# Performance work log

Hardware: AMD Instinct MI355X
Metric: run time of the kernel (lower is better)

## Reference

```python
import jax, jax.numpy as jnp
import numpy as np

NMS_THR = 0.3


def pairwise_iou(b):
    # b: [N,4] in x1,y1,x2,y2
    area = (b[:, 2] - b[:, 0]) * (b[:, 3] - b[:, 1])  # [N]
    x1 = jnp.maximum(b[:, None, 0], b[None, :, 0])
    y1 = jnp.maximum(b[:, None, 1], b[None, :, 1])
    x2 = jnp.minimum(b[:, None, 2], b[None, :, 2])
    y2 = jnp.minimum(b[:, None, 3], b[None, :, 3])
    inter = jnp.clip(x2 - x1, 0.0) * jnp.clip(y2 - y1, 0.0)
    return inter / (area[:, None] + area[None, :] - inter + 1e-9)


def nms_keep(boxes, scores, valid, thr):
    # greedy NMS, fixed-shape: returns bool keep mask in original order
    N = boxes.shape[0]
    order = jnp.argsort(-jnp.where(valid, scores, -jnp.inf))
    b = boxes[order]
    v = valid[order]
    iou = pairwise_iou(b)  # [N,N]

    def step(keep, i):
        suppressed = jnp.any(keep & (iou[i] > thr))
        keep = keep.at[i].set(v[i] & jnp.logical_not(suppressed))
        return keep, None

    keep_sorted, _ = jax.lax.scan(step, jnp.zeros((N,), dtype=bool), jnp.arange(N))
    return jnp.zeros((N,), dtype=bool).at[order].set(keep_sorted)


def setup_inputs() -> dict:
    key = jax.random.key(0)
    k1, k2, k3, k4 = jax.random.split(key, 4)
    N, C, S = 6000, 81, 800
    # well-formed proposals: x1,y1 in [0, 600), w,h in [8, 200)
    xy = jax.random.uniform(k1, (N, 2), dtype=jnp.float32) * 600.0
    wh = 8.0 + jax.random.uniform(k2, (N, 2), dtype=jnp.float32) * 192.0
    proposals = jnp.concatenate([xy, xy + wh], axis=1)  # [N,4]
    reg = jax.random.normal(k3, (N, C * 4), dtype=jnp.float32)
    clss = jax.random.normal(k4, (N, C), dtype=jnp.float32) * 2.0
    stds = jnp.array([0.1, 0.1, 0.2, 0.2], dtype=jnp.float32)
    return {"proposals": proposals, "reg": reg, "clss": clss, "stds": stds, "img_size": S}


def reference(proposals, reg, clss, stds, img_size):
    N, C = clss.shape
    # anchors_bbox2offset: x1y1x2y2 -> center x,y + w,h
    w = proposals[:, 2] - proposals[:, 0]
    h = proposals[:, 3] - proposals[:, 1]
    cx = proposals[:, 0] + 0.5 * w
    cy = proposals[:, 1] + 0.5 * h
    # class selection
    probs = jax.nn.softmax(clss, axis=1)
    cls_idx = jnp.argmax(probs, axis=1)  # [N]
    score = jnp.take_along_axis(probs, cls_idx[:, None], axis=1)[:, 0]
    valid = cls_idx != 0  # non-background
    reg4 = reg.reshape(N, C, 4)
    t = jnp.take_along_axis(reg4, cls_idx[:, None, None], axis=1)[:, 0, :] * stds  # [N,4]
    # decode
    px = cx + w * t[:, 0]
    py = cy + h * t[:, 1]
    pw = w * jnp.exp(t[:, 2])
    ph = h * jnp.exp(t[:, 3])
    # offset2bbox + clip
    hi = jnp.float32(img_size - 1)
    x1 = jnp.clip(px - 0.5 * pw, 0.0, hi)
    y1 = jnp.clip(py - 0.5 * ph, 0.0, hi)
    x2 = jnp.clip(px + 0.5 * pw, 0.0, hi)
    y2 = jnp.clip(py + 0.5 * ph, 0.0, hi)
    boxes = jnp.stack((x1, y1, x2, y2), axis=1)  # [N,4]
    keep = nms_keep(jax.lax.stop_gradient(boxes), jax.lax.stop_gradient(score), valid, NMS_THR)
    m = keep.astype(boxes.dtype)
    return boxes * m[:, None], score * m, cls_idx * keep.astype(cls_idx.dtype)
```

## Files before the change

### kernel.cpp

```cpp
#include <hip/hip_runtime.h>
#include <math.h>

#define NMS_THR 0.3f
#define NACC 8

__device__ __forceinline__ float fmul(float a, float b){ return __fmul_rn(a,b); }
__device__ __forceinline__ float fadd(float a, float b){ return __fadd_rn(a,b); }
__device__ __forceinline__ float fsub(float a, float b){ return __fsub_rn(a,b); }

#define BAR_LDS() asm volatile("s_waitcnt lgkmcnt(0)\n\ts_barrier" ::: "memory")

__device__ __forceinline__ unsigned long long rdlane64(unsigned long long v, int a) {
    unsigned long long l = (unsigned int)__builtin_amdgcn_readlane((int)(unsigned int)v, a);
    unsigned long long h = (unsigned int)__builtin_amdgcn_readlane((int)(unsigned int)(v >> 32), a);
    return (h << 32) | l;
}
__device__ __forceinline__ unsigned long long rfl64(unsigned long long x){
    unsigned int lo = (unsigned int)__builtin_amdgcn_readfirstlane((int)(unsigned int)x);
    unsigned int hi = (unsigned int)__builtin_amdgcn_readfirstlane((int)(unsigned int)(x >> 32));
    return ((unsigned long long)hi << 32) | lo;
}

__global__ __launch_bounds__(256) void k_decode(
    const float* __restrict__ prop, const float* __restrict__ reg,
    const float* __restrict__ clss, const float* __restrict__ stds,
    const int* __restrict__ imgsz,
    float* __restrict__ boxes, float* __restrict__ key,
    float* __restrict__ score, int* __restrict__ cls,
    int N, int C)
{
    int wid  = threadIdx.x >> 6;
    int lane = threadIdx.x & 63;
    int n = blockIdx.x * 4 + wid;
    if (n >= N) return;
    const float* row = clss + (long)n * C;
    float ninf = -__builtin_inff();
    float x0 = (lane < C)      ? row[lane]      : ninf;
    float x1 = (lane + 64 < C) ? row[lane + 64] : ninf;
    float m = fmaxf(x0, x1);
    for (int o = 32; o > 0; o >>= 1) m = fmaxf(m, __shfl_xor(m, o));
    float e0 = (lane < C)      ? expf(x0 - m) : 0.0f;
    float e1 = (lane + 64 < C) ? expf(x1 - m) : 0.0f;
    float s = e0 + e1;
    for (int o = 32; o > 0; o >>= 1) s += __shfl_xor(s, o);
    float bv; int bi;
    if (e0 >= e1) { bv = e0; bi = lane; } else { bv = e1; bi = lane + 64; }
    for (int o = 32; o > 0; o >>= 1) {
        float ov = __shfl_xor(bv, o);
        int   oi = __shfl_xor(bi, o);
        if (ov > bv || (ov == bv && oi < bi)) { bv = ov; bi = oi; }
    }
    if (lane == 0) {
        float sc = 1.0f / s;
        int   c  = bi;
        int   valid = (c != 0);
        float p0 = prop[n*4+0], p1 = prop[n*4+1], p2 = prop[n*4+2], p3 = prop[n*4+3];
        float w  = fsub(p2, p0), h = fsub(p3, p1);
        float cx = fadd(p0, fmul(0.5f, w));
        float cy = fadd(p1, fmul(0.5f, h));
        const float* rr = reg + (long)n * C * 4 + (long)c * 4;
        float t0 = fmul(rr[0], stds[0]);
        float t1 = fmul(rr[1], stds[1]);
        float t2 = fmul(rr[2], stds[2]);
        float t3 = fmul(rr[3], stds[3]);
        float px = fadd(cx, fmul(w, t0));
        float py = fadd(cy, fmul(h, t1));
        float pw = fmul(w, expf(t2));
        float ph = fmul(h, expf(t3));
        float hi = (float)(imgsz[0] - 1);
        float bx1 = fminf(fmaxf(fsub(px, fmul(0.5f, pw)), 0.0f), hi);
        float by1 = fminf(fmaxf(fsub(py, fmul(0.5f, ph)), 0.0f), hi);
        float bx2 = fminf(fmaxf(fadd(px, fmul(0.5f, pw)), 0.0f), hi);
        float by2 = fminf(fmaxf(fadd(py, fmul(0.5f, ph)), 0.0f), hi);
        boxes[n*4+0]=bx1; boxes[n*4+1]=by1; boxes[n*4+2]=bx2; boxes[n*4+3]=by2;
        score[n] = sc;
        cls[n]   = c;
        key[n]   = valid ? sc : ninf;
    }
}

__global__ __launch_bounds__(256) void k_rank(
    const float* __restrict__ key, const float* __restrict__ boxes,
    float* __restrict__ boxesSorted, float* __restrict__ areaSorted,
    float* __restrict__ keySorted, int* __restrict__ rank,
    int* __restrict__ nValidPtr, int N)
{
    extern __shared__ float lkey[];
    __shared__ int part[256];
    int tid = threadIdx.x;
    for (int j = tid; j < N; j += 256) lkey[j] = key[j];
    __syncthreads();

    int i = blockIdx.x * 64 + (tid & 63);
    int s = tid >> 6;
    int Q = (N + 3) >> 2;
    int r_part = 0;
    if (i < N) {
        float ki = lkey[i];
        int j0 = s * Q, j1 = min(N, j0 + Q);
        for (int j = j0; j < j1; ++j) {
            float kj = lkey[j];
            r_part += (kj > ki) || (kj == ki && j < i);
        }
    }
    part[tid] = r_part;
    __syncthreads();

    if (tid < 64 && i < N) {
        int r = part[tid] + part[tid+64] + part[tid+128] + part[tid+192];
        float ki = lkey[i];
        rank[i] = r;
        float b0 = boxes[i*4+0], b1 = boxes[i*4+1], b2 = boxes[i*4+2], b3 = boxes[i*4+3];
        boxesSorted[r*4+0]=b0; boxesSorted[r*4+1]=b1; boxesSorted[r*4+2]=b2; boxesSorted[r*4+3]=b3;
        areaSorted[r] = fmul(fsub(b2,b0), fsub(b3,b1));
        keySorted[r]  = ki;
    }

    if (blockIdx.x == 0) {
        __syncthreads();
        float ninf = -__builtin_inff();
        int inv = 0;
        for (int j = tid; j < N; j += 256) inv += (lkey[j] == ninf);
        part[tid] = inv;
        __syncthreads();
        if (tid == 0) {
            int t = 0;
            for (int q = 0; q < 256; ++q) t += part[q];
            nValidPtr[0] = N - t;
        }
    }
}

__global__ __launch_bounds__(256) void k_mask(
    const float* __restrict__ bs, const float* __restrict__ areas,
    const float* __restrict__ keySorted, unsigned long long* __restrict__ mask,
    unsigned long long* __restrict__ dq,
    int N, int W, int Wpad)
{
    int wid  = threadIdx.x >> 6;
    int lane = threadIdx.x & 63;
    int i = blockIdx.x * 4 + wid;
    if (i >= N) return;
    if (keySorted[i] == -__builtin_inff()) return;
    float ax1 = bs[i*4+0], ay1 = bs[i*4+1], ax2 = bs[i*4+2], ay2 = bs[i*4+3];
    float aa  = areas[i];
    int w0 = i >> 6;
    if (lane == 0) {
        dq[i*4+0] = 0ULL; dq[i*4+1] = 0ULL; dq[i*4+2] = 0ULL; dq[i*4+3] = 0ULL;
    }
    for (int w = w0; w < W; ++w) {
        int j = w*64 + lane;
        int bit = 0;
        if (j < N && j > i) {
            float bx1 = bs[j*4+0], by1 = bs[j*4+1], bx2 = bs[j*4+2], by2 = bs[j*4+3];
            float ba  = areas[j];
            float ix1 = fmaxf(ax1,bx1), iy1 = fmaxf(ay1,by1);
            float ix2 = fminf(ax2,bx2), iy2 = fminf(ay2,by2);
            float iw = fmaxf(fsub(ix2,ix1), 0.0f);
            float ih = fmaxf(fsub(iy2,iy1), 0.0f);
            float inter = fmul(iw, ih);
            float denom = fadd(fsub(fadd(aa, ba), inter), 1e-9f);
            float iou = inter / denom;
            bit = (iou > NMS_THR) ? 1 : 0;
        }
        unsigned long long bm = __ballot(bit);
        if (lane == 0) {
            mask[(long)i*Wpad + w] = bm;
            int d = w - w0;
            if (d < 4) dq[i*4+d] = bm;
        }
    }
}

__global__ __launch_bounds__((NACC+1)*64, 1) void k_scan(
    const unsigned long long* __restrict__ mask,
    const unsigned long long* __restrict__ dq,
    const int* __restrict__ nValidPtr,
    int* __restrict__ keepSorted, int N, int W, int Wpad)
{
    __shared__ unsigned long long ldsPartA[NACC+1];
    __shared__ unsigned long long ldsPartB[NACC+1];
    __shared__ unsigned long long ldsKeepLo, ldsKeepHi;
    int tid  = threadIdx.x;
    int wid  = tid >> 6;
    int lane = tid & 63;
    for (int i = tid; i < N; i += (NACC+1)*64) keepSorted[i] = 0;
    if (tid <= NACC) { ldsPartA[tid] = 0ULL; ldsPartB[tid] = 0ULL; }
    if (tid == 0) { ldsKeepLo = 0ULL; ldsKeepHi = 0ULL; }
    __syncthreads();

    int nValid  = __builtin_amdgcn_readfirstlane(nValidPtr[0]);
    int nChunks = (nValid + 127) >> 7;

    unsigned long long A0=0,A1=0,A2=0,A3=0,B0=0,B1=0,B2=0,B3=0;
    unsigned long long sacc_prevA = 0ULL, sacc_prevB = 0ULL;
    if (wid == 0) {
        int rA = lane, rB = 64 + lane;
        if (rA < N && nChunks > 0) {
            ulonglong2 a01 = *(const ulonglong2*)(dq + (size_t)rA*4);
            ulonglong2 a23 = *(const ulonglong2*)(dq + (size_t)rA*4 + 2);
            A0=a01.x; A1=a01.y; A2=a23.x; A3=a23.y;
        }
        if (rB < N && nChunks > 0) {
            ulonglong2 b01 = *(const ulonglong2*)(dq + (size_t)rB*4);
            ulonglong2 b23 = *(const ulonglong2*)(dq + (size_t)rB*4 + 2);
            B0=b01.x; B1=b01.y; B2=b23.x; B3=b23.y;
        }
    }
    unsigned long long accx = 0ULL, accy = 0ULL;
    bool accWave = (wid >= 1);
    int  accIdx  = wid - 1;
    bool laneok  = (2*lane + 1 < Wpad);

    for (int c = 0; c < nChunks; ++c) {
        int base = c << 7;
        if (wid == 0) {
            unsigned long long nA0=0,nA1=0,nA2=0,nA3=0,nB0=0,nB1=0,nB2=0,nB3=0;
            if (c + 1 < nChunks) {
                int rA = base + 128 + lane, rB = base + 192 + lane;
                if (rA < N) {
                    ulonglong2 a01 = *(const ulonglong2*)(dq + (size_t)rA*4);
                    ulonglong2 a23 = *(const ulonglong2*)(dq + (size_t)rA*4 + 2);
                    nA0=a01.x; nA1=a01.y; nA2=a23.x; nA3=a23.y;
                }
                if (rB < N) {
                    ulonglong2 b01 = *(const ulonglong2*)(dq + (size_t)rB*4);
                    ulonglong2 b23 = *(const ulonglong2*)(dq + (size_t)rB*4 + 2);
                    nB0=b01.x; nB1=b01.y; nB2=b23.x; nB3=b23.y;
                }
            }

            unsigned long long pA = sacc_prevA, pB = sacc_prevB;
#pragma unroll
            for (int k = 1; k <= NACC; ++k) { pA |= ldsPartA[k]; pB |= ldsPartB[k]; }
            unsigned long long incLo = rfl64(pA), incHi = rfl64(pB);
            int nv  = nValid - base;
            unsigned long long validLo = (nv >= 64) ? ~0ULL : ((1ULL << nv) - 1ULL);
            int nv2 = nv - 64;
            unsigned long long validHi = (nv2 >= 64) ? ~0ULL
                                        : (nv2 <= 0 ? 0ULL : ((1ULL << nv2) - 1ULL));
            unsigned long long candLo = validLo & ~incLo;
            unsigned long long candHi = validHi & ~incHi;
            unsigned long long keepLo = 0ULL, keepHi = 0ULL, sA = 0ULL, sB = 0ULL;
            while (candLo) {
                int a = __builtin_ctzll(candLo);
                keepLo |= 1ULL << a;
                unsigned long long dFH = rdlane64(A0, a);
                unsigned long long dSH = rdlane64(A1, a);
                sA |= rdlane64(A2, a);
                sB |= rdlane64(A3, a);
                candLo &= ~(1ULL << a) & ~dFH;
                candHi &= ~dSH;
            }
            while (candHi) {
                int a = __builtin_ctzll(candHi);
                keepHi |= 1ULL << a;
                unsigned long long dSH = rdlane64(B0, a);
                sA |= rdlane64(B1, a);
                sB |= rdlane64(B2, a);
                candHi &= ~(1ULL << a) & ~dSH;
            }
            sacc_prevA = sA; sacc_prevB = sB;
            if (lane == 0) { ldsKeepLo = keepLo; ldsKeepHi = keepHi; }
            if (base + lane < N)      keepSorted[base + lane]      = (int)((keepLo >> lane) & 1ULL);
            if (base + 64 + lane < N) keepSorted[base + 64 + lane] = (int)((keepHi >> lane) & 1ULL);
            A0=nA0; A1=nA1; A2=nA2; A3=nA3; B0=nB0; B1=nB1; B2=nB2; B3=nB3;
        }
        BAR_LDS();
        unsigned long long kLo = ldsKeepLo;
        unsigned long long kHi = ldsKeepHi;
        if (accWave && laneok && lane == c + 1) {
            ldsPartA[wid] = accx;
            ldsPartB[wid] = accy;
        }
        BAR_LDS();
        if (accWave && laneok) {
            unsigned int myb = (accIdx < 4)
                ? (unsigned int)((kLo >> (16*accIdx)) & 0xFFFFULL)
                : (unsigned int)((kHi >> (16*(accIdx-4))) & 0xFFFFULL);
            if (myb) {
                const unsigned long long* mb =
                    mask + (size_t)(base + 16*accIdx) * Wpad + 2*lane;
                unsigned int b = myb;
                int a0 = __builtin_ctz(b); b &= b - 1;
                int a1 = -1, a2 = -1, a3 = -1;
                if (b) { a1 = __builtin_ctz(b); b &= b - 1; }
                if (b) { a2 = __builtin_ctz(b); b &= b - 1; }
                if (b) { a3 = __builtin_ctz(b); b &= b - 1; }
                ulonglong2 v0 = {0,0}, v1 = {0,0}, v2 = {0,0}, v3 = {0,0};
                v0 = *(const ulonglong2*)(mb + (size_t)a0 * Wpad);
                if (a1 >= 0) v1 = *(const ulonglong2*)(mb + (size_t)a1 * Wpad);
                if (a2 >= 0) v2 = *(const ulonglong2*)(mb + (size_t)a2 * Wpad);
                if (a3 >= 0) v3 = *(const ulonglong2*)(mb + (size_t)a3 * Wpad);
                accx |= (v0.x | v1.x) | (v2.x | v3.x);
                accy |= (v0.y | v1.y) | (v2.y | v3.y);
                while (b) {
                    int a = __builtin_ctz(b); b &= b - 1;
                    ulonglong2 v = *(const ulonglong2*)(mb + (size_t)a * Wpad);
                    accx |= v.x; accy |= v.y;
                }
            }
        }
    }
}

__global__ __launch_bounds__(256) void k_out(
    const float* __restrict__ boxes, const float* __restrict__ score,
    const int* __restrict__ cls, const int* __restrict__ rank,
    const int* __restrict__ keepSorted,
    float* __restrict__ out, int N)
{
    int n = blockIdx.x * blockDim.x + threadIdx.x;
    if (n >= N) return;
    int k = keepSorted[rank[n]];
    float m = (float)k;
    out[n*4+0] = boxes[n*4+0]*m;
    out[n*4+1] = boxes[n*4+1]*m;
    out[n*4+2] = boxes[n*4+2]*m;
    out[n*4+3] = boxes[n*4+3]*m;
    out[(long)N*4 + n] = score[n]*m;
    out[(long)N*5 + n] = (float)(cls[n] * k);
}

extern "C" void kernel_launch(void* const* d_in, const int* in_sizes, int n_in,
                              void* d_out, int out_size, void* d_ws, size_t ws_size,
                              hipStream_t stream) {
    const float* prop = (const float*)d_in[0];
    const float* reg  = (const float*)d_in[1];
    const float* clss = (const float*)d_in[2];
    const float* stds = (const float*)d_in[3];
    const int*   img  = (const int*)d_in[4];

    int N = in_sizes[0] / 4;
    int C = in_sizes[2] / N;
    int W = (N + 63) / 64;
    int Wpad = (W + 1) & ~1;

    char* ws = (char*)d_ws;
    size_t off = 0;
    float* boxes       = (float*)(ws + off); off += (size_t)N*4*sizeof(float);
    float* key         = (float*)(ws + off); off += (size_t)N*sizeof(float);
    float* score       = (float*)(ws + off); off += (size_t)N*sizeof(float);
    int*   cls         = (int*)  (ws + off); off += (size_t)N*sizeof(int);
    int*   rank        = (int*)  (ws + off); off += (size_t)N*sizeof(int);
    float* boxesSorted = (float*)(ws + off); off += (size_t)N*4*sizeof(float);
    float* areaSorted  = (float*)(ws + off); off += (size_t)N*sizeof(float);
    float* keySorted   = (float*)(ws + off); off += (size_t)N*sizeof(float);
    int*   keepSorted  = (int*)  (ws + off); off += (size_t)N*sizeof(int);
    int*   nValid      = (int*)  (ws + off); off += sizeof(int);
    off = (off + 31) & ~(size_t)31;
    unsigned long long* dq    = (unsigned long long*)(ws + off);
    off += (size_t)N * 4 * sizeof(unsigned long long);
    unsigned long long* mask  = (unsigned long long*)(ws + off);
    off += (size_t)N * Wpad * sizeof(unsigned long long);
    (void)ws_size; (void)out_size; (void)n_in;

    int rowBlocks  = (N + 3) / 4;
    int thrBlocks  = (N + 255) / 256;
    int rankBlocks = (N + 63) / 64;

    k_decode<<<rowBlocks, 256, 0, stream>>>(prop, reg, clss, stds, img,
                                            boxes, key, score, cls, N, C);
    k_rank<<<rankBlocks, 256, (size_t)N*sizeof(float), stream>>>(key, boxes,
                                            boxesSorted, areaSorted, keySorted, rank, nValid, N);
    k_mask<<<rowBlocks, 256, 0, stream>>>(boxesSorted, areaSorted, keySorted,
                                          mask, dq, N, W, Wpad);
    k_scan<<<1, (NACC+1)*64, 0, stream>>>(mask, dq, nValid, keepSorted, N, W, Wpad);
    k_out<<<thrBlocks, 256, 0, stream>>>(boxes, score, cls, rank, keepSorted,
                                         (float*)d_out, N);
}
```

Baseline: 184.7 us.

## Reduce NMS scan serial chain with LDS atomic-or slot and deferred keep writes

The per-chunk reduction of accumulator partials moves from an 8-entry LDS read loop to a single LDS slot that accumulator waves atomically OR into. Wave 0 reads and clears that slot. The greedy inner loop now tracks only in-chunk suppression; the cross-half and future-chunk masks are gathered afterwards only over the kept bits, which shortens the serial dependency chain. Keep bits are buffered in LDS and written to global memory once at the end instead of per chunk. The buffer holds 128 entries, which limits N to 8192, and the atomics add LDS contention.

Result: slower. 260.9 us (+41.3%).

```diff
diff --git a/kernel.cpp b/kernel.cpp
--- a/kernel.cpp
+++ b/kernel.cpp
@@ -178,15 +178,13 @@
     const int* __restrict__ nValidPtr,
     int* __restrict__ keepSorted, int N, int W, int Wpad)
 {
-    __shared__ unsigned long long ldsPartA[NACC+1];
-    __shared__ unsigned long long ldsPartB[NACC+1];
-    __shared__ unsigned long long ldsKeepLo, ldsKeepHi;
+    __shared__ unsigned long long ldsSlotA, ldsSlotB;
+    __shared__ unsigned long long ldsKeepBuf[128];
     int tid  = threadIdx.x;
     int wid  = tid >> 6;
     int lane = tid & 63;
-    for (int i = tid; i < N; i += (NACC+1)*64) keepSorted[i] = 0;
-    if (tid <= NACC) { ldsPartA[tid] = 0ULL; ldsPartB[tid] = 0ULL; }
-    if (tid == 0) { ldsKeepLo = 0ULL; ldsKeepHi = 0ULL; }
+    for (int i = tid; i < 128; i += (NACC+1)*64) ldsKeepBuf[i] = 0ULL;
+    if (tid == 0) { ldsSlotA = 0ULL; ldsSlotB = 0ULL; }
     __syncthreads();
 
     int nValid  = __builtin_amdgcn_readfirstlane(nValidPtr[0]);
@@ -194,14 +192,14 @@
 
     unsigned long long A0=0,A1=0,A2=0,A3=0,B0=0,B1=0,B2=0,B3=0;
     unsigned long long sacc_prevA = 0ULL, sacc_prevB = 0ULL;
-    if (wid == 0) {
+    if (wid == 0 && nChunks > 0) {
         int rA = lane, rB = 64 + lane;
-        if (rA < N && nChunks > 0) {
+        if (rA < N) {
             ulonglong2 a01 = *(const ulonglong2*)(dq + (size_t)rA*4);
             ulonglong2 a23 = *(const ulonglong2*)(dq + (size_t)rA*4 + 2);
             A0=a01.x; A1=a01.y; A2=a23.x; A3=a23.y;
         }
-        if (rB < N && nChunks > 0) {
+        if (rB < N) {
             ulonglong2 b01 = *(const ulonglong2*)(dq + (size_t)rB*4);
             ulonglong2 b23 = *(const ulonglong2*)(dq + (size_t)rB*4 + 2);
             B0=b01.x; B1=b01.y; B2=b23.x; B3=b23.y;
@@ -230,10 +228,10 @@
                 }
             }
 
-            unsigned long long pA = sacc_prevA, pB = sacc_prevB;
-#pragma unroll
-            for (int k = 1; k <= NACC; ++k) { pA |= ldsPartA[k]; pB |= ldsPartB[k]; }
-            unsigned long long incLo = rfl64(pA), incHi = rfl64(pB);
+            unsigned long long pA = ldsSlotA, pB = ldsSlotB;
+            if (lane == 0) { ldsSlotA = 0ULL; ldsSlotB = 0ULL; }
+            unsigned long long incLo = rfl64(pA) | sacc_prevA;
+            unsigned long long incHi = rfl64(pB) | sacc_prevB;
             int nv  = nValid - base;
             unsigned long long validLo = (nv >= 64) ? ~0ULL : ((1ULL << nv) - 1ULL);
             int nv2 = nv - 64;
@@ -241,37 +239,52 @@
                                         : (nv2 <= 0 ? 0ULL : ((1ULL << nv2) - 1ULL));
             unsigned long long candLo = validLo & ~incLo;
             unsigned long long candHi = validHi & ~incHi;
-            unsigned long long keepLo = 0ULL, keepHi = 0ULL, sA = 0ULL, sB = 0ULL;
+            unsigned long long keepLo = 0ULL, keepHi = 0ULL;
+
             while (candLo) {
                 int a = __builtin_ctzll(candLo);
-                keepLo |= 1ULL << a;
-                unsigned long long dFH = rdlane64(A0, a);
-                unsigned long long dSH = rdlane64(A1, a);
-                sA |= rdlane64(A2, a);
-                sB |= rdlane64(A3, a);
-                candLo &= ~(1ULL << a) & ~dFH;
-                candHi &= ~dSH;
-            }
+                unsigned long long bit = 1ULL << a;
+                keepLo |= bit;
+                candLo &= ~bit & ~rdlane64(A0, a);
+            }
+            unsigned long long mHi = 0ULL, sA = 0ULL, sB = 0ULL;
+            {
+                unsigned long long kb = keepLo;
+                while (kb) {
+                    int a = __builtin_ctzll(kb); kb &= kb - 1ULL;
+                    mHi |= rdlane64(A1, a);
+                    sA  |= rdlane64(A2, a);
+                    sB  |= rdlane64(A3, a);
+                }
+            }
+            candHi &= ~mHi;
             while (candHi) {
                 int a = __builtin_ctzll(candHi);
-                keepHi |= 1ULL << a;
-                unsigned long long dSH = rdlane64(B0, a);
-                sA |= rdlane64(B1, a);
-                sB |= rdlane64(B2, a);
-                candHi &= ~(1ULL << a) & ~dSH;
+                unsigned long long bit = 1ULL << a;
+                keepHi |= bit;
+                candHi &= ~bit & ~rdlane64(B0, a);
+            }
+            {
+                unsigned long long kb = keepHi;
+                while (kb) {
+                    int a = __builtin_ctzll(kb); kb &= kb - 1ULL;
+                    sA |= rdlane64(B1, a);
+                    sB |= rdlane64(B2, a);
+                }
             }
             sacc_prevA = sA; sacc_prevB = sB;
-            if (lane == 0) { ldsKeepLo = keepLo; ldsKeepHi = keepHi; }
-            if (base + lane < N)      keepSorted[base + lane]      = (int)((keepLo >> lane) & 1ULL);
-            if (base + 64 + lane < N) keepSorted[base + 64 + lane] = (int)((keepHi >> lane) & 1ULL);
+            if (lane == 0) {
+                ldsKeepBuf[2*c]     = keepLo;
+                ldsKeepBuf[2*c + 1] = keepHi;
+            }
             A0=nA0; A1=nA1; A2=nA2; A3=nA3; B0=nB0; B1=nB1; B2=nB2; B3=nB3;
         }
         BAR_LDS();
-        unsigned long long kLo = ldsKeepLo;
-        unsigned long long kHi = ldsKeepHi;
+        unsigned long long kLo = ldsKeepBuf[2*c];
+        unsigned long long kHi = ldsKeepBuf[2*c + 1];
         if (accWave && laneok && lane == c + 1) {
-            ldsPartA[wid] = accx;
-            ldsPartB[wid] = accy;
+            atomicOr(&ldsSlotA, accx);
+            atomicOr(&ldsSlotB, accy);
         }
         BAR_LDS();
         if (accWave && laneok) {
@@ -302,6 +315,9 @@
             }
         }
     }
+    __syncthreads();
+    for (int i = tid; i < N; i += (NACC+1)*64)
+        keepSorted[i] = (int)((ldsKeepBuf[i >> 6] >> (i & 63)) & 1ULL);
 }
 
 __global__ __launch_bounds__(256) void k_out(
```

## Fuse output kernel into NMS scan and batch suppression ORs via wave reductions

Applied to the files above, without the earlier changes.

Removes the separate output kernel and has the single-block scan kernel write the masked boxes, scores and classes after its final barrier, saving one launch. Inside the serial greedy loop, the per-kept-box readlanes for the far-chunk suppression words are taken off the critical path. Those contributions are instead gathered once per chunk with lane-select plus butterfly OR reductions. The cost is that the output writes now run on a single block of 576 threads instead of many blocks, and each chunk adds a few shuffle reductions.

Measured after the change: 200.5 us. 8.6% more time.

```diff
diff --git a/kernel.cpp b/kernel.cpp
--- a/kernel.cpp
+++ b/kernel.cpp
@@ -19,6 +19,10 @@
     unsigned int lo = (unsigned int)__builtin_amdgcn_readfirstlane((int)(unsigned int)x);
     unsigned int hi = (unsigned int)__builtin_amdgcn_readfirstlane((int)(unsigned int)(x >> 32));
     return ((unsigned long long)hi << 32) | lo;
+}
+__device__ __forceinline__ unsigned long long waveOr64(unsigned long long v){
+    for (int o = 32; o > 0; o >>= 1) v |= __shfl_xor(v, o);
+    return v;
 }
 
 __global__ __launch_bounds__(256) void k_decode(
@@ -176,7 +180,11 @@
     const unsigned long long* __restrict__ mask,
     const unsigned long long* __restrict__ dq,
     const int* __restrict__ nValidPtr,
-    int* __restrict__ keepSorted, int N, int W, int Wpad)
+    int* __restrict__ keepSorted,
+    const float* __restrict__ boxes, const float* __restrict__ score,
+    const int* __restrict__ cls, const int* __restrict__ rank,
+    float* __restrict__ out,
+    int N, int W, int Wpad)
 {
     __shared__ unsigned long long ldsPartA[NACC+1];
     __shared__ unsigned long long ldsPartB[NACC+1];
@@ -194,14 +202,14 @@
 
     unsigned long long A0=0,A1=0,A2=0,A3=0,B0=0,B1=0,B2=0,B3=0;
     unsigned long long sacc_prevA = 0ULL, sacc_prevB = 0ULL;
-    if (wid == 0) {
+    if (wid == 0 && nChunks > 0) {
         int rA = lane, rB = 64 + lane;
-        if (rA < N && nChunks > 0) {
+        if (rA < N) {
             ulonglong2 a01 = *(const ulonglong2*)(dq + (size_t)rA*4);
             ulonglong2 a23 = *(const ulonglong2*)(dq + (size_t)rA*4 + 2);
             A0=a01.x; A1=a01.y; A2=a23.x; A3=a23.y;
         }
-        if (rB < N && nChunks > 0) {
+        if (rB < N) {
             ulonglong2 b01 = *(const ulonglong2*)(dq + (size_t)rB*4);
             ulonglong2 b23 = *(const ulonglong2*)(dq + (size_t)rB*4 + 2);
             B0=b01.x; B1=b01.y; B2=b23.x; B3=b23.y;
@@ -241,26 +249,32 @@
                                         : (nv2 <= 0 ? 0ULL : ((1ULL << nv2) - 1ULL));
             unsigned long long candLo = validLo & ~incLo;
             unsigned long long candHi = validHi & ~incHi;
-            unsigned long long keepLo = 0ULL, keepHi = 0ULL, sA = 0ULL, sB = 0ULL;
+            unsigned long long keepLo = 0ULL, keepHi = 0ULL;
+
             while (candLo) {
                 int a = __builtin_ctzll(candLo);
-                keepLo |= 1ULL << a;
-                unsigned long long dFH = rdlane64(A0, a);
-                unsigned long long dSH = rdlane64(A1, a);
-                sA |= rdlane64(A2, a);
-                sB |= rdlane64(A3, a);
-                candLo &= ~(1ULL << a) & ~dFH;
-                candHi &= ~dSH;
+                unsigned long long bit = 1ULL << a;
+                keepLo |= bit;
+                candLo &= ~bit & ~rdlane64(A0, a);
+            }
+            {
+                unsigned long long sel = ((keepLo >> lane) & 1ULL) ? A1 : 0ULL;
+                candHi &= ~waveOr64(sel);
             }
             while (candHi) {
                 int a = __builtin_ctzll(candHi);
-                keepHi |= 1ULL << a;
-                unsigned long long dSH = rdlane64(B0, a);
-                sA |= rdlane64(B1, a);
-                sB |= rdlane64(B2, a);
-                candHi &= ~(1ULL << a) & ~dSH;
-            }
-            sacc_prevA = sA; sacc_prevB = sB;
+                unsigned long long bit = 1ULL << a;
+                keepHi |= bit;
+                candHi &= ~bit & ~rdlane64(B0, a);
+            }
+            {
+                unsigned long long kL = (keepLo >> lane) & 1ULL;
+                unsigned long long kH = (keepHi >> lane) & 1ULL;
+                unsigned long long selA = (kL ? A2 : 0ULL) | (kH ? B1 : 0ULL);
+                unsigned long long selB = (kL ? A3 : 0ULL) | (kH ? B2 : 0ULL);
+                sacc_prevA = waveOr64(selA);
+                sacc_prevB = waveOr64(selB);
+            }
             if (lane == 0) { ldsKeepLo = keepLo; ldsKeepHi = keepHi; }
             if (base + lane < N)      keepSorted[base + lane]      = (int)((keepLo >> lane) & 1ULL);
             if (base + 64 + lane < N) keepSorted[base + 64 + lane] = (int)((keepHi >> lane) & 1ULL);
@@ -302,24 +316,18 @@
             }
         }
     }
-}
-
-__global__ __launch_bounds__(256) void k_out(
-    const float* __restrict__ boxes, const float* __restrict__ score,
-    const int* __restrict__ cls, const int* __restrict__ rank,
-    const int* __restrict__ keepSorted,
-    float* __restrict__ out, int N)
-{
-    int n = blockIdx.x * blockDim.x + threadIdx.x;
-    if (n >= N) return;
-    int k = keepSorted[rank[n]];
-    float m = (float)k;
-    out[n*4+0] = boxes[n*4+0]*m;
-    out[n*4+1] = boxes[n*4+1]*m;
-    out[n*4+2] = boxes[n*4+2]*m;
-    out[n*4+3] = boxes[n*4+3]*m;
-    out[(long)N*4 + n] = score[n]*m;
-    out[(long)N*5 + n] = (float)(cls[n] * k);
+
+    __syncthreads();
+    for (int n = tid; n < N; n += (NACC+1)*64) {
+        int k = keepSorted[rank[n]];
+        float m = (float)k;
+        out[n*4+0] = boxes[n*4+0]*m;
+        out[n*4+1] = boxes[n*4+1]*m;
+        out[n*4+2] = boxes[n*4+2]*m;
+        out[n*4+3] = boxes[n*4+3]*m;
+        out[(long)N*4 + n] = score[n]*m;
+        out[(long)N*5 + n] = (float)(cls[n] * k);
+    }
 }
 
 extern "C" void kernel_launch(void* const* d_in, const int* in_sizes, int n_in,
@@ -356,7 +364,6 @@
     (void)ws_size; (void)out_size; (void)n_in;
 
     int rowBlocks  = (N + 3) / 4;
-    int thrBlocks  = (N + 255) / 256;
     int rankBlocks = (N + 63) / 64;
 
     k_decode<<<rowBlocks, 256, 0, stream>>>(prop, reg, clss, stds, img,
@@ -365,7 +372,7 @@
                                             boxesSorted, areaSorted, keySorted, rank, nValid, N);
     k_mask<<<rowBlocks, 256, 0, stream>>>(boxesSorted, areaSorted, keySorted,
                                           mask, dq, N, W, Wpad);
-    k_scan<<<1, (NACC+1)*64, 0, stream>>>(mask, dq, nValid, keepSorted, N, W, Wpad);
-    k_out<<<thrBlocks, 256, 0, stream>>>(boxes, score, cls, rank, keepSorted,
-                                         (float*)d_out, N);
-}
+    k_scan<<<1, (NACC+1)*64, 0, stream>>>(mask, dq, nValid, keepSorted,
+                                          boxes, score, cls, rank, (float*)d_out,
+                                          N, W, Wpad);
+}
```
